# Performance work log

Measured on AMD Instinct MI355X. Metric: run time of the kernel, lower is better.

## Reference

```python
import jax, jax.numpy as jnp
import numpy as np

NUM_HEADS = 16
NUM_KV_HEADS = 4
HEAD_DIM = 128
WINDOW = 1024  # sliding window: key j visible to query i iff 0 <= i - j <= WINDOW
SCALE = 0.08838834764831845  # 1/sqrt(HEAD_DIM)
NEG_INF = -1e30


def setup_inputs() -> dict:
    key = jax.random.key(0)
    k1, k2, k3, k4 = jax.random.split(key, 4)
    B, S = 4, 2048
    T = B * S
    return {
        "q": jax.random.normal(k1, (T, NUM_HEADS * HEAD_DIM), dtype=jnp.float32),
        "k": jax.random.normal(k2, (T, NUM_KV_HEADS * HEAD_DIM), dtype=jnp.float32),
        "v": jax.random.normal(k3, (T, NUM_KV_HEADS * HEAD_DIM), dtype=jnp.float32),
        "sinks": jax.random.normal(k4, (NUM_HEADS,), dtype=jnp.float32),
        "batch": B,
        "seqlen": S,
    }


def reference(q, k, v, sinks, batch, seqlen):
    """Varlen causal sliding-window attention with learnable per-head sink logits.

    Equal-length sequences: total_tokens = batch * seqlen, matching
    cu_seqlens = [0, S, 2S, ...] in flash_attn_varlen_func.
    """
    B, S = batch, seqlen
    g = NUM_HEADS // NUM_KV_HEADS
    q = q.reshape(B, S, NUM_HEADS, HEAD_DIM)
    k = k.reshape(B, S, NUM_KV_HEADS, HEAD_DIM)
    v = v.reshape(B, S, NUM_KV_HEADS, HEAD_DIM)
    # GQA: expand kv heads to match query heads
    k = jnp.repeat(k, g, axis=2)  # [B,S,H,D]
    v = jnp.repeat(v, g, axis=2)

    logits = jnp.einsum("bqhd,bkhd->bhqk", q, k) * SCALE  # [B,H,S,S]

    i = jnp.arange(S)[:, None]
    j = jnp.arange(S)[None, :]
    mask = (j <= i) & ((i - j) <= WINDOW)  # causal + sliding window (left=WINDOW, right=-1)
    logits = jnp.where(mask, logits, NEG_INF)

    # Learnable sink: one extra virtual logit per head, contributing no value.
    sink_col = jnp.broadcast_to(sinks[None, :, None, None], (B, NUM_HEADS, S, 1))
    logits = jnp.concatenate([logits, sink_col], axis=-1)  # [B,H,S,S+1]
    probs = jax.nn.softmax(logits, axis=-1)[..., :S]  # drop sink prob (value = 0)

    o = jnp.einsum("bhqk,bkhd->bqhd", probs, v)  # [B,S,H,D]
    return o.reshape(B * S, NUM_HEADS * HEAD_DIM)
```

## Files before the change

### kernel.cpp

```cpp
#include <hip/hip_runtime.h>
#include <hip/hip_bf16.h>

#define NH    16
#define NKVH  4
#define HD    128
#define WIN   1024
#define SEQ   2048
#define NB    4
#define QROW  (NH * HD)
#define KROW  (NKVH * HD)
#define LOG2E 1.4426950408889634f
#define QSC   (0.08838834764831845f * LOG2E)

#define KSTR 136
#define VSTR 40

typedef __attribute__((ext_vector_type(8))) short short8;
typedef __attribute__((ext_vector_type(4))) float float4v;

__device__ __forceinline__ unsigned short f2bf(float f) {
    unsigned int u = __float_as_uint(f);
    unsigned int r = (u + 0x7FFFu + ((u >> 16) & 1u)) >> 16;
    return (unsigned short)r;
}

__device__ __forceinline__ unsigned int pk2bf(float a, float b) {
    float2 t; t.x = a; t.y = b;
    __hip_bfloat162 h = __float22bfloat162_rn(t);
    union { __hip_bfloat162 h; unsigned int u; } cv;
    cv.h = h;
    return cv.u;
}

__global__ __launch_bounds__(256)
void cvt_k_kernel(const float* __restrict__ kg, unsigned short* __restrict__ kb) {
    const size_t idx = ((size_t)blockIdx.x * 256 + threadIdx.x) * 8;
    float4 a = *(const float4*)(kg + idx);
    float4 b = *(const float4*)(kg + idx + 4);
    uint4 w;
    w.x = pk2bf(a.x, a.y); w.y = pk2bf(a.z, a.w);
    w.z = pk2bf(b.x, b.y); w.w = pk2bf(b.z, b.w);
    *(uint4*)(kb + idx) = w;
}

#define VTSTR 72
__global__ __launch_bounds__(256)
void cvt_vt_kernel(const float* __restrict__ vg, unsigned short* __restrict__ vt) {
    __shared__ unsigned short T[128 * VTSTR];
    const int blk = blockIdx.x;
    const int b   = blk >> 7;
    const int kvh = (blk >> 5) & 3;
    const int kb  = blk & 31;
    const int t   = threadIdx.x;

    const int klocal = t >> 2;
    const int d0     = (t & 3) * 32;
    const float* src = vg + (size_t)(b * SEQ + kb * 64 + klocal) * KROW + kvh * HD + d0;
#pragma unroll
    for (int c = 0; c < 8; ++c) {
        float4 x = *(const float4*)(src + c * 4);
        T[(d0 + c * 4 + 0) * VTSTR + klocal] = f2bf(x.x);
        T[(d0 + c * 4 + 1) * VTSTR + klocal] = f2bf(x.y);
        T[(d0 + c * 4 + 2) * VTSTR + klocal] = f2bf(x.z);
        T[(d0 + c * 4 + 3) * VTSTR + klocal] = f2bf(x.w);
    }
    __syncthreads();

    const int d    = t >> 1;
    const int half = t & 1;
    const unsigned short* s = &T[d * VTSTR + half * 32];
    unsigned short* dst = vt + ((size_t)((b * NKVH + kvh) * HD) + d) * SEQ + kb * 64 + half * 32;
#pragma unroll
    for (int c = 0; c < 4; ++c)
        *(uint4*)(dst + c * 8) = *(const uint4*)(s + c * 8);
}

__global__ __launch_bounds__(256, 3)
void attn_swa_sink_kernel(const float* __restrict__ qg,
                          const unsigned short* __restrict__ kb,
                          const unsigned short* __restrict__ vt,
                          const float* __restrict__ sinks,
                          float* __restrict__ og) {
    __shared__ __align__(16) unsigned short Klds[32 * KSTR];
    __shared__ __align__(16) unsigned short Vlds[128 * VSTR];

    const int gid  = blockIdx.x;
    const int xcd  = gid & 7;
    const int rest = gid >> 3;
    const int qt   = rest >> 1;
    const int g    = ((rest & 1) << 3) | xcd;
    const int b    = g >> 2;
    const int kvh  = g & 3;

    const int tid  = threadIdx.x;
    const int wave = tid >> 6;
    const int lane = tid & 63;
    const int l15  = lane & 15;
    const int quad = lane >> 4;
    const int h    = kvh * 4 + wave;
    const int q0   = qt * 32;

    const float* qbase = qg + (size_t)(b * SEQ) * QROW;
    const unsigned short* kbase = kb + (size_t)(b * SEQ) * KROW + kvh * HD;
    const unsigned short* vtbase = vt + (size_t)((b * NKVH + kvh) * HD) * SEQ;

    short8 qf[2][4];
#pragma unroll
    for (int qs = 0; qs < 2; ++qs) {
        const float* qr = qbase + (size_t)(q0 + qs * 16 + l15) * QROW + h * HD + quad * 8;
#pragma unroll
        for (int c = 0; c < 4; ++c) {
            float4 x = *(const float4*)(qr + c * 32);
            float4 y = *(const float4*)(qr + c * 32 + 4);
            union { unsigned int u[4]; short8 s; } cv;
            cv.u[0] = pk2bf(x.x * QSC, x.y * QSC);
            cv.u[1] = pk2bf(x.z * QSC, x.w * QSC);
            cv.u[2] = pk2bf(y.x * QSC, y.y * QSC);
            cv.u[3] = pk2bf(y.z * QSC, y.w * QSC);
            qf[qs][c] = cv.s;
        }
    }

    const float sinkv = sinks[h] * LOG2E;
    float m_i[2] = { sinkv, sinkv };
    float l_i[2] = { 1.0f, 1.0f };
    float4v accO[2][8];
#pragma unroll
    for (int qs = 0; qs < 2; ++qs)
#pragma unroll
        for (int f = 0; f < 8; ++f) accO[qs][f] = (float4v)0.0f;

    const int kr  = tid >> 3, kcg = tid & 7;
    const int lrow = ((kr & 1) << 4) | (kr >> 1);
    const int vd  = tid >> 1, vh = tid & 1;

    int kt0 = q0 - WIN; if (kt0 < 0) kt0 = 0;
    const int kend = q0 + 32;

    uint4 kpre0, kpre1, vpre0, vpre1;
    {
        const unsigned short* kp = kbase + (size_t)(kt0 + kr) * KROW + kcg * 16;
        kpre0 = *(const uint4*)(kp);
        kpre1 = *(const uint4*)(kp + 8);
        const unsigned short* vp = vtbase + (size_t)vd * SEQ + kt0 + vh * 16;
        vpre0 = *(const uint4*)(vp);
        vpre1 = *(const uint4*)(vp + 8);
    }

    for (int k0 = kt0; k0 < kend; k0 += 32) {
        __syncthreads();
        *(uint4*)&Klds[lrow * KSTR + kcg * 16]     = kpre0;
        *(uint4*)&Klds[lrow * KSTR + kcg * 16 + 8] = kpre1;
        *(uint4*)&Vlds[vd * VSTR + vh * 16]        = vpre0;
        *(uint4*)&Vlds[vd * VSTR + vh * 16 + 8]    = vpre1;
        if (k0 + 32 < kend) {
            const unsigned short* kp = kbase + (size_t)(k0 + 32 + kr) * KROW + kcg * 16;
            kpre0 = *(const uint4*)(kp);
            kpre1 = *(const uint4*)(kp + 8);
            const unsigned short* vp = vtbase + (size_t)vd * SEQ + (k0 + 32) + vh * 16;
            vpre0 = *(const uint4*)(vp);
            vpre1 = *(const uint4*)(vp + 8);
        }
        __syncthreads();

        float4v sacc[2][2];
        sacc[0][0] = (float4v)0.0f; sacc[0][1] = (float4v)0.0f;
        sacc[1][0] = (float4v)0.0f; sacc[1][1] = (float4v)0.0f;
#pragma unroll
        for (int c = 0; c < 4; ++c) {
            short8 kf0 = *(const short8*)&Klds[(l15)      * KSTR + c * 32 + quad * 8];
            short8 kf1 = *(const short8*)&Klds[(16 + l15) * KSTR + c * 32 + quad * 8];
            sacc[0][0] = __builtin_amdgcn_mfma_f32_16x16x32_bf16(kf0, qf[0][c], sacc[0][0], 0, 0, 0);
            sacc[0][1] = __builtin_amdgcn_mfma_f32_16x16x32_bf16(kf0, qf[1][c], sacc[0][1], 0, 0, 0);
            sacc[1][0] = __builtin_amdgcn_mfma_f32_16x16x32_bf16(kf1, qf[0][c], sacc[1][0], 0, 0, 0);
            sacc[1][1] = __builtin_amdgcn_mfma_f32_16x16x32_bf16(kf1, qf[1][c], sacc[1][1], 0, 0, 0);
        }

        short8 pf[2];
#pragma unroll
        for (int qs = 0; qs < 2; ++qs) {
            const int query = q0 + qs * 16 + l15;
            const bool full = (k0 + 31 <= q0 + qs * 16) && (q0 + qs * 16 + 15 - k0 <= WIN);
            float ps[2][4];
            float mx = -3.0e38f;
            if (full) {
#pragma unroll
                for (int ks = 0; ks < 2; ++ks)
#pragma unroll
                    for (int r = 0; r < 4; ++r) {
                        float s = sacc[ks][qs][r];
                        ps[ks][r] = s;
                        mx = fmaxf(mx, s);
                    }
            } else {
#pragma unroll
                for (int ks = 0; ks < 2; ++ks)
#pragma unroll
                    for (int r = 0; r < 4; ++r) {
                        const int key = k0 + 8 * quad + 2 * r + ks;
                        const unsigned d = (unsigned)(query - key);
                        float s = (d <= WIN) ? sacc[ks][qs][r] : -1.0e30f;
                        ps[ks][r] = s;
                        mx = fmaxf(mx, s);
                    }
            }
            mx = fmaxf(mx, __shfl_xor(mx, 16));
            mx = fmaxf(mx, __shfl_xor(mx, 32));
            const float mold = m_i[qs];
            const float mnew = fmaxf(mold, mx);
            m_i[qs] = mnew;
            float sum = 0.0f;
            union { unsigned int u[4]; short8 s; } cv;
#pragma unroll
            for (int r = 0; r < 4; ++r) {
                const float p0 = exp2f(ps[0][r] - mnew);
                const float p1 = exp2f(ps[1][r] - mnew);
                sum += p0 + p1;
                cv.u[r] = pk2bf(p0, p1);
            }
            pf[qs] = cv.s;
            sum += __shfl_xor(sum, 16);
            sum += __shfl_xor(sum, 32);
            if (__any(mnew > mold)) {
                const float alpha = exp2f(mold - mnew);
                l_i[qs] = l_i[qs] * alpha + sum;
#pragma unroll
                for (int r = 0; r < 4; ++r) {
                    const float ar = __shfl(alpha, quad * 4 + r);
#pragma unroll
                    for (int f = 0; f < 8; ++f) accO[qs][f][r] *= ar;
                }
            } else {
                l_i[qs] += sum;
            }
        }

#pragma unroll
        for (int f = 0; f < 8; ++f) {
            short8 vf = *(const short8*)&Vlds[(f * 16 + l15) * VSTR + quad * 8];
            accO[0][f] = __builtin_amdgcn_mfma_f32_16x16x32_bf16(pf[0], vf, accO[0][f], 0, 0, 0);
            accO[1][f] = __builtin_amdgcn_mfma_f32_16x16x32_bf16(pf[1], vf, accO[1][f], 0, 0, 0);
        }
    }

    float* obase = og + (size_t)(b * SEQ) * QROW + h * HD;
#pragma unroll
    for (int qs = 0; qs < 2; ++qs) {
#pragma unroll
        for (int r = 0; r < 4; ++r) {
            const float lq  = __shfl(l_i[qs], quad * 4 + r);
            const float inv = __builtin_amdgcn_rcpf(lq);
            float* orow = obase + (size_t)(q0 + qs * 16 + quad * 4 + r) * QROW;
#pragma unroll
            for (int f = 0; f < 8; ++f)
                orow[f * 16 + l15] = accO[qs][f][r] * inv;
        }
    }
}

extern "C" void kernel_launch(void* const* d_in, const int* in_sizes, int n_in,
                              void* d_out, int out_size, void* d_ws, size_t ws_size,
                              hipStream_t stream) {
    const float* q     = (const float*)d_in[0];
    const float* k     = (const float*)d_in[1];
    const float* v     = (const float*)d_in[2];
    const float* sinks = (const float*)d_in[3];
    float* o = (float*)d_out;

    unsigned short* kb = (unsigned short*)d_ws;
    unsigned short* vt = kb + (size_t)NB * SEQ * KROW;

    cvt_k_kernel<<<dim3(NB * SEQ * KROW / (256 * 8)), dim3(256), 0, stream>>>(k, kb);
    cvt_vt_kernel<<<dim3(NB * NKVH * (SEQ / 64)), dim3(256), 0, stream>>>(v, vt);

    attn_swa_sink_kernel<<<dim3(NB * NKVH * (SEQ / 32)), dim3(256), 0, stream>>>(
        q, kb, vt, sinks, o);
}
```

Before: 244.1 us.

## Double query tile to 64 rows per block, reverse tile order, raise MFMA priority

```diff
diff --git a/kernel.cpp b/kernel.cpp
--- a/kernel.cpp
+++ b/kernel.cpp
@@ -75,7 +75,7 @@
         *(uint4*)(dst + c * 8) = *(const uint4*)(s + c * 8);
 }
 
-__global__ __launch_bounds__(256, 3)
+__global__ __launch_bounds__(256, 2)
 void attn_swa_sink_kernel(const float* __restrict__ qg,
                           const unsigned short* __restrict__ kb,
                           const unsigned short* __restrict__ vt,
@@ -87,7 +87,7 @@
     const int gid  = blockIdx.x;
     const int xcd  = gid & 7;
     const int rest = gid >> 3;
-    const int qt   = rest >> 1;
+    const int qt   = 31 - (rest >> 1);
     const int g    = ((rest & 1) << 3) | xcd;
     const int b    = g >> 2;
     const int kvh  = g & 3;
@@ -98,15 +98,15 @@
     const int l15  = lane & 15;
     const int quad = lane >> 4;
     const int h    = kvh * 4 + wave;
-    const int q0   = qt * 32;
+    const int q0   = qt * 64;
 
     const float* qbase = qg + (size_t)(b * SEQ) * QROW;
     const unsigned short* kbase = kb + (size_t)(b * SEQ) * KROW + kvh * HD;
     const unsigned short* vtbase = vt + (size_t)((b * NKVH + kvh) * HD) * SEQ;
 
-    short8 qf[2][4];
-#pragma unroll
-    for (int qs = 0; qs < 2; ++qs) {
+    short8 qf[4][4];
+#pragma unroll
+    for (int qs = 0; qs < 4; ++qs) {
         const float* qr = qbase + (size_t)(q0 + qs * 16 + l15) * QROW + h * HD + quad * 8;
 #pragma unroll
         for (int c = 0; c < 4; ++c) {
@@ -122,11 +122,11 @@
     }
 
     const float sinkv = sinks[h] * LOG2E;
-    float m_i[2] = { sinkv, sinkv };
-    float l_i[2] = { 1.0f, 1.0f };
-    float4v accO[2][8];
-#pragma unroll
-    for (int qs = 0; qs < 2; ++qs)
+    float m_i[4] = { sinkv, sinkv, sinkv, sinkv };
+    float l_i[4] = { 1.0f, 1.0f, 1.0f, 1.0f };
+    float4v accO[4][8];
+#pragma unroll
+    for (int qs = 0; qs < 4; ++qs)
 #pragma unroll
         for (int f = 0; f < 8; ++f) accO[qs][f] = (float4v)0.0f;
 
@@ -135,7 +135,7 @@
     const int vd  = tid >> 1, vh = tid & 1;
 
     int kt0 = q0 - WIN; if (kt0 < 0) kt0 = 0;
-    const int kend = q0 + 32;
+    const int kend = q0 + 64;
 
     uint4 kpre0, kpre1, vpre0, vpre1;
     {
@@ -163,22 +163,27 @@
         }
         __syncthreads();
 
-        float4v sacc[2][2];
-        sacc[0][0] = (float4v)0.0f; sacc[0][1] = (float4v)0.0f;
-        sacc[1][0] = (float4v)0.0f; sacc[1][1] = (float4v)0.0f;
+        float4v sacc[2][4];
+#pragma unroll
+        for (int ks = 0; ks < 2; ++ks)
+#pragma unroll
+            for (int qs = 0; qs < 4; ++qs) sacc[ks][qs] = (float4v)0.0f;
+        __builtin_amdgcn_s_setprio(1);
 #pragma unroll
         for (int c = 0; c < 4; ++c) {
             short8 kf0 = *(const short8*)&Klds[(l15)      * KSTR + c * 32 + quad * 8];
             short8 kf1 = *(const short8*)&Klds[(16 + l15) * KSTR + c * 32 + quad * 8];
-            sacc[0][0] = __builtin_amdgcn_mfma_f32_16x16x32_bf16(kf0, qf[0][c], sacc[0][0], 0, 0, 0);
-            sacc[0][1] = __builtin_amdgcn_mfma_f32_16x16x32_bf16(kf0, qf[1][c], sacc[0][1], 0, 0, 0);
-            sacc[1][0] = __builtin_amdgcn_mfma_f32_16x16x32_bf16(kf1, qf[0][c], sacc[1][0], 0, 0, 0);
-            sacc[1][1] = __builtin_amdgcn_mfma_f32_16x16x32_bf16(kf1, qf[1][c], sacc[1][1], 0, 0, 0);
-        }
-
-        short8 pf[2];
-#pragma unroll
-        for (int qs = 0; qs < 2; ++qs) {
+#pragma unroll
+            for (int qs = 0; qs < 4; ++qs) {
+                sacc[0][qs] = __builtin_amdgcn_mfma_f32_16x16x32_bf16(kf0, qf[qs][c], sacc[0][qs], 0, 0, 0);
+                sacc[1][qs] = __builtin_amdgcn_mfma_f32_16x16x32_bf16(kf1, qf[qs][c], sacc[1][qs], 0, 0, 0);
+            }
+        }
+        __builtin_amdgcn_s_setprio(0);
+
+        short8 pf[4];
+#pragma unroll
+        for (int qs = 0; qs < 4; ++qs) {
             const int query = q0 + qs * 16 + l15;
             const bool full = (k0 + 31 <= q0 + qs * 16) && (q0 + qs * 16 + 15 - k0 <= WIN);
             float ps[2][4];
@@ -235,17 +240,20 @@
             }
         }
 
+        __builtin_amdgcn_s_setprio(1);
 #pragma unroll
         for (int f = 0; f < 8; ++f) {
             short8 vf = *(const short8*)&Vlds[(f * 16 + l15) * VSTR + quad * 8];
-            accO[0][f] = __builtin_amdgcn_mfma_f32_16x16x32_bf16(pf[0], vf, accO[0][f], 0, 0, 0);
-            accO[1][f] = __builtin_amdgcn_mfma_f32_16x16x32_bf16(pf[1], vf, accO[1][f], 0, 0, 0);
-        }
+#pragma unroll
+            for (int qs = 0; qs < 4; ++qs)
+                accO[qs][f] = __builtin_amdgcn_mfma_f32_16x16x32_bf16(pf[qs], vf, accO[qs][f], 0, 0, 0);
+        }
+        __builtin_amdgcn_s_setprio(0);
     }
 
     float* obase = og + (size_t)(b * SEQ) * QROW + h * HD;
 #pragma unroll
-    for (int qs = 0; qs < 2; ++qs) {
+    for (int qs = 0; qs < 4; ++qs) {
 #pragma unroll
         for (int r = 0; r < 4; ++r) {
             const float lq  = __shfl(l_i[qs], quad * 4 + r);
@@ -273,6 +281,6 @@
     cvt_k_kernel<<<dim3(NB * SEQ * KROW / (256 * 8)), dim3(256), 0, stream>>>(k, kb);
     cvt_vt_kernel<<<dim3(NB * NKVH * (SEQ / 64)), dim3(256), 0, stream>>>(v, vt);
 
-    attn_swa_sink_kernel<<<dim3(NB * NKVH * (SEQ / 32)), dim3(256), 0, stream>>>(
+    attn_swa_sink_kernel<<<dim3(NB * NKVH * (SEQ / 64)), dim3(256), 0, stream>>>(
         q, kb, vt, sinks, o);
 }
```

After: 352.8 us. 1.45x slower.

## Double-buffer K/V LDS tiles, defer softmax rescale, reverse tile order

Applied to the files above, without the earlier changes.

```diff
diff --git a/kernel.cpp b/kernel.cpp
--- a/kernel.cpp
+++ b/kernel.cpp
@@ -11,6 +11,7 @@
 #define KROW  (NKVH * HD)
 #define LOG2E 1.4426950408889634f
 #define QSC   (0.08838834764831845f * LOG2E)
+#define DTHR  8.0f
 
 #define KSTR 136
 #define VSTR 40
@@ -81,13 +82,13 @@
                           const unsigned short* __restrict__ vt,
                           const float* __restrict__ sinks,
                           float* __restrict__ og) {
-    __shared__ __align__(16) unsigned short Klds[32 * KSTR];
-    __shared__ __align__(16) unsigned short Vlds[128 * VSTR];
+    __shared__ __align__(16) unsigned short Klds[2][32 * KSTR];
+    __shared__ __align__(16) unsigned short Vlds[2][128 * VSTR];
 
     const int gid  = blockIdx.x;
     const int xcd  = gid & 7;
     const int rest = gid >> 3;
-    const int qt   = rest >> 1;
+    const int qt   = 63 - (rest >> 1);
     const int g    = ((rest & 1) << 3) | xcd;
     const int b    = g >> 2;
     const int kvh  = g & 3;
@@ -123,7 +124,7 @@
 
     const float sinkv = sinks[h] * LOG2E;
     float m_i[2] = { sinkv, sinkv };
-    float l_i[2] = { 1.0f, 1.0f };
+    float l_i[2] = { 0.0f, 0.0f };
     float4v accO[2][8];
 #pragma unroll
     for (int qs = 0; qs < 2; ++qs)
@@ -136,6 +137,9 @@
 
     int kt0 = q0 - WIN; if (kt0 < 0) kt0 = 0;
     const int kend = q0 + 32;
+
+    const int koff = lrow * KSTR + kcg * 16;
+    const int voff = vd * VSTR + vh * 16;
 
     uint4 kpre0, kpre1, vpre0, vpre1;
     {
@@ -147,12 +151,13 @@
         vpre1 = *(const uint4*)(vp + 8);
     }
 
-    for (int k0 = kt0; k0 < kend; k0 += 32) {
+    int pp = 0;
+    for (int k0 = kt0; k0 < kend; k0 += 32, pp ^= 1) {
+        *(uint4*)&Klds[pp][koff]     = kpre0;
+        *(uint4*)&Klds[pp][koff + 8] = kpre1;
+        *(uint4*)&Vlds[pp][voff]     = vpre0;
+        *(uint4*)&Vlds[pp][voff + 8] = vpre1;
         __syncthreads();
-        *(uint4*)&Klds[lrow * KSTR + kcg * 16]     = kpre0;
-        *(uint4*)&Klds[lrow * KSTR + kcg * 16 + 8] = kpre1;
-        *(uint4*)&Vlds[vd * VSTR + vh * 16]        = vpre0;
-        *(uint4*)&Vlds[vd * VSTR + vh * 16 + 8]    = vpre1;
         if (k0 + 32 < kend) {
             const unsigned short* kp = kbase + (size_t)(k0 + 32 + kr) * KROW + kcg * 16;
             kpre0 = *(const uint4*)(kp);
@@ -161,20 +166,21 @@
             vpre0 = *(const uint4*)(vp);
             vpre1 = *(const uint4*)(vp + 8);
         }
-        __syncthreads();
 
         float4v sacc[2][2];
         sacc[0][0] = (float4v)0.0f; sacc[0][1] = (float4v)0.0f;
         sacc[1][0] = (float4v)0.0f; sacc[1][1] = (float4v)0.0f;
+        __builtin_amdgcn_s_setprio(1);
 #pragma unroll
         for (int c = 0; c < 4; ++c) {
-            short8 kf0 = *(const short8*)&Klds[(l15)      * KSTR + c * 32 + quad * 8];
-            short8 kf1 = *(const short8*)&Klds[(16 + l15) * KSTR + c * 32 + quad * 8];
+            short8 kf0 = *(const short8*)&Klds[pp][(l15)      * KSTR + c * 32 + quad * 8];
+            short8 kf1 = *(const short8*)&Klds[pp][(16 + l15) * KSTR + c * 32 + quad * 8];
             sacc[0][0] = __builtin_amdgcn_mfma_f32_16x16x32_bf16(kf0, qf[0][c], sacc[0][0], 0, 0, 0);
             sacc[0][1] = __builtin_amdgcn_mfma_f32_16x16x32_bf16(kf0, qf[1][c], sacc[0][1], 0, 0, 0);
             sacc[1][0] = __builtin_amdgcn_mfma_f32_16x16x32_bf16(kf1, qf[0][c], sacc[1][0], 0, 0, 0);
             sacc[1][1] = __builtin_amdgcn_mfma_f32_16x16x32_bf16(kf1, qf[1][c], sacc[1][1], 0, 0, 0);
         }
+        __builtin_amdgcn_s_setprio(0);
 
         short8 pf[2];
 #pragma unroll
@@ -207,8 +213,19 @@
             mx = fmaxf(mx, __shfl_xor(mx, 16));
             mx = fmaxf(mx, __shfl_xor(mx, 32));
             const float mold = m_i[qs];
-            const float mnew = fmaxf(mold, mx);
-            m_i[qs] = mnew;
+            float mnew = mold;
+            if (__any(mx > mold + DTHR)) {
+                mnew = fmaxf(mold, mx);
+                m_i[qs] = mnew;
+                const float alpha = exp2f(mold - mnew);
+                l_i[qs] *= alpha;
+#pragma unroll
+                for (int r = 0; r < 4; ++r) {
+                    const float ar = __shfl(alpha, quad * 4 + r);
+#pragma unroll
+                    for (int f = 0; f < 8; ++f) accO[qs][f][r] *= ar;
+                }
+            }
             float sum = 0.0f;
             union { unsigned int u[4]; short8 s; } cv;
 #pragma unroll
@@ -218,37 +235,30 @@
                 sum += p0 + p1;
                 cv.u[r] = pk2bf(p0, p1);
             }
+            l_i[qs] += sum;
             pf[qs] = cv.s;
-            sum += __shfl_xor(sum, 16);
-            sum += __shfl_xor(sum, 32);
-            if (__any(mnew > mold)) {
-                const float alpha = exp2f(mold - mnew);
-                l_i[qs] = l_i[qs] * alpha + sum;
-#pragma unroll
-                for (int r = 0; r < 4; ++r) {
-                    const float ar = __shfl(alpha, quad * 4 + r);
-#pragma unroll
-                    for (int f = 0; f < 8; ++f) accO[qs][f][r] *= ar;
-                }
-            } else {
-                l_i[qs] += sum;
-            }
-        }
-
+        }
+
+        __builtin_amdgcn_s_setprio(1);
 #pragma unroll
         for (int f = 0; f < 8; ++f) {
-            short8 vf = *(const short8*)&Vlds[(f * 16 + l15) * VSTR + quad * 8];
+            short8 vf = *(const short8*)&Vlds[pp][(f * 16 + l15) * VSTR + quad * 8];
             accO[0][f] = __builtin_amdgcn_mfma_f32_16x16x32_bf16(pf[0], vf, accO[0][f], 0, 0, 0);
             accO[1][f] = __builtin_amdgcn_mfma_f32_16x16x32_bf16(pf[1], vf, accO[1][f], 0, 0, 0);
         }
+        __builtin_amdgcn_s_setprio(0);
     }
 
     float* obase = og + (size_t)(b * SEQ) * QROW + h * HD;
 #pragma unroll
     for (int qs = 0; qs < 2; ++qs) {
+        float l = l_i[qs];
+        l += __shfl_xor(l, 16);
+        l += __shfl_xor(l, 32);
+        l += exp2f(sinkv - m_i[qs]);
 #pragma unroll
         for (int r = 0; r < 4; ++r) {
-            const float lq  = __shfl(l_i[qs], quad * 4 + r);
+            const float lq  = __shfl(l, quad * 4 + r);
             const float inv = __builtin_amdgcn_rcpf(lq);
             float* orow = obase + (size_t)(q0 + qs * 16 + quad * 4 + r) * QROW;
 #pragma unroll
```

After: 225.0 us. 1.09x faster.
